# Kernel tuning notes

Measured on AMD Instinct MI355X. Metric: run time of the kernel, lower is better.

Reference implementation:

```python
import jax, jax.numpy as jnp
import numpy as np

B, L, D, H = 2, 4096, 512, 8
DK = D // H
SCALE = 1.0 / float(np.sqrt(DK))


def setup_inputs() -> dict:
    key = jax.random.key(0)
    k1, k2, k3 = jax.random.split(key, 3)
    x = jax.random.normal(k1, (B, L, D), dtype=jnp.float32)
    w_qkv = jax.random.normal(k2, (3 * D, D), dtype=jnp.float32) * 0.02
    w_o = jax.random.normal(k3, (D, D), dtype=jnp.float32) * 0.02
    return {"x": x, "w_qkv": w_qkv, "w_o": w_o}


def reference(x, w_qkv, w_o):
    b, l, d = x.shape
    # qkv projection: Linear(d, 3d, bias=False) -> x @ W^T
    qkv = (x @ w_qkv.T).reshape(b, l, 3, H, DK).transpose(2, 0, 3, 1, 4)  # [3,B,H,L,dk]
    q, k, v = qkv[0], qkv[1], qkv[2]
    # naive O(L^2) attention (faithful to source)
    scores = jnp.einsum("bhld,bhmd->bhlm", q, k) * SCALE  # [B,H,L,L]
    attn = jax.nn.softmax(scores, axis=-1)
    ctx = jnp.einsum("bhlm,bhmd->bhld", attn, v)  # [B,H,L,dk]
    ctx = ctx.transpose(0, 2, 1, 3).reshape(b, l, d)
    return ctx @ w_o.T
```

## Files before the change

kernel.cpp:

```cpp
#include <hip/hip_runtime.h>


#define Bq 2
#define Lq 4096
#define Dq 512
#define Hq 8
#define DKq 64
#define PST 40

using short8  = __attribute__((ext_vector_type(8))) short;
using ushort8 = __attribute__((ext_vector_type(8))) unsigned short;
using float4v = __attribute__((ext_vector_type(4))) float;
using half4   = __attribute__((ext_vector_type(4))) _Float16;
typedef unsigned short u16;
typedef unsigned int   u32;

__device__ __forceinline__ u16 f2bf(float f) {
    u32 u = __float_as_uint(f);
    u += 0x7fffu + ((u >> 16) & 1u);
    return (u16)(u >> 16);
}

__device__ __forceinline__ float4v mfma16(short8 a, short8 b, float4v c) {
    return __builtin_amdgcn_mfma_f32_16x16x32_bf16(a, b, c, 0, 0, 0);
}

__device__ __forceinline__ void gload_lds16(const u16* g, u16* l) {
    __builtin_amdgcn_global_load_lds(
        (const __attribute__((address_space(1))) unsigned int*)g,
        (__attribute__((address_space(3))) unsigned int*)l,
        16, 0, 0);
}

__global__ __launch_bounds__(256) void castall(const float* __restrict__ x,
                                               const float* __restrict__ wq,
                                               const float* __restrict__ wo,
                                               u16* __restrict__ xb,
                                               u16* __restrict__ wqb,
                                               u16* __restrict__ wob) {
    int g = blockIdx.x;
    const float* s; u16* d; int base;
    if (g < 4096)      { s = x;  d = xb;  base = g * 1024; }
    else if (g < 4864) { s = wq; d = wqb; base = (g - 4096) * 1024; }
    else               { s = wo; d = wob; base = (g - 4864) * 1024; }
    int i = base + threadIdx.x * 4;
    float4 f = *(const float4*)&s[i];
    ushort4 o;
    o.x = f2bf(f.x); o.y = f2bf(f.y); o.z = f2bf(f.z); o.w = f2bf(f.w);
    *(ushort4*)&d[i] = o;
}

__global__ __launch_bounds__(256) void qkv_gemm(const u16* __restrict__ A,
                                                const u16* __restrict__ Bw,
                                                u16* __restrict__ qb,
                                                u16* __restrict__ kb,
                                                u16* __restrict__ vt) {
    __shared__ __align__(16) union {
        struct { u16 A[128 * 64]; u16 B[128 * 64]; } s;
        u16 epi[128 * 134];
    } sm;
    const int m0 = blockIdx.x * 128, n0 = blockIdx.y * 128;
    const int tid = threadIdx.x, w = tid >> 6, lane = tid & 63;
    const int l15 = lane & 15, quad = lane >> 4;
    const int wy = w & 1, wx = w >> 1;
    const int r8 = lane >> 3, c8 = lane & 7, csw = c8 ^ r8;
    const int sw = l15 & 7;

    float4v acc[4][4];
    float4v zero = {0.f, 0.f, 0.f, 0.f};
#pragma unroll
    for (int mi = 0; mi < 4; mi++)
#pragma unroll
        for (int ni = 0; ni < 4; ni++) acc[mi][ni] = zero;

    for (int k0 = 0; k0 < 512; k0 += 64) {
#pragma unroll
        for (int i = 0; i < 4; i++) {
            int row = w * 32 + i * 8;
            gload_lds16(&A[(size_t)(m0 + row + r8) * 512 + k0 + csw * 8], &sm.s.A[row * 64]);
            gload_lds16(&Bw[(size_t)(n0 + row + r8) * 512 + k0 + csw * 8], &sm.s.B[row * 64]);
        }
        __syncthreads();
        short8 af0[4], af1[4], bf0[4], bf1[4];
#pragma unroll
        for (int t = 0; t < 4; t++) {
            int rowA = wy * 64 + t * 16 + l15;
            af0[t] = *(const short8*)&sm.s.A[rowA * 64 + ((quad ^ sw) * 8)];
            af1[t] = *(const short8*)&sm.s.A[rowA * 64 + (((quad + 4) ^ sw) * 8)];
            int rowB = wx * 64 + t * 16 + l15;
            bf0[t] = *(const short8*)&sm.s.B[rowB * 64 + ((quad ^ sw) * 8)];
            bf1[t] = *(const short8*)&sm.s.B[rowB * 64 + (((quad + 4) ^ sw) * 8)];
        }
#pragma unroll
        for (int mi = 0; mi < 4; mi++)
#pragma unroll
            for (int ni = 0; ni < 4; ni++) {
                acc[mi][ni] = mfma16(af0[mi], bf0[ni], acc[mi][ni]);
                acc[mi][ni] = mfma16(af1[mi], bf1[ni], acc[mi][ni]);
            }
        __syncthreads();
    }

    const int sel = n0 >> 9;
    if (sel < 2) {
        const float sc = (sel == 0) ? 0.125f : 1.0f;
#pragma unroll
        for (int mi = 0; mi < 4; mi++)
#pragma unroll
            for (int ni = 0; ni < 4; ni++)
#pragma unroll
                for (int r = 0; r < 4; r++)
                    sm.epi[(wy * 64 + mi * 16 + quad * 4 + r) * 134 + wx * 64 + ni * 16 + l15] =
                        f2bf(acc[mi][ni][r] * sc);
        __syncthreads();
        u16* tgt = (sel == 0) ? qb : kb;
#pragma unroll
        for (int i = 0; i < 8; i++) {
            int flat = i * 2048 + tid * 8;
            int row = flat >> 7, col = flat & 127;
            ushort8 vv = *(const ushort8*)&sm.epi[row * 134 + col];
            int dg = (n0 & 511) + col, h = dg >> 6, dk = dg & 63;
            int mm = m0 + row, b = mm >> 12, l = mm & 4095;
            *(ushort8*)&tgt[((size_t)(b * Hq + h) * Lq + l) * DKq + dk] = vv;
        }
    } else {
#pragma unroll
        for (int mi = 0; mi < 4; mi++)
#pragma unroll
            for (int ni = 0; ni < 4; ni++) {
                ushort4 v4;
                v4.x = f2bf(acc[mi][ni][0]); v4.y = f2bf(acc[mi][ni][1]);
                v4.z = f2bf(acc[mi][ni][2]); v4.w = f2bf(acc[mi][ni][3]);
                *(ushort4*)&sm.epi[(wx * 64 + ni * 16 + l15) * 134 + wy * 64 + mi * 16 + quad * 4] = v4;
            }
        __syncthreads();
#pragma unroll
        for (int i = 0; i < 8; i++) {
            int flat = i * 2048 + tid * 8;
            int vrow = flat >> 7, vcol = flat & 127;
            ushort8 vv = *(const ushort8*)&sm.epi[vrow * 134 + vcol];
            int dg = (n0 & 511) + vrow, h = dg >> 6, dk = dg & 63;
            int mm = m0 + vcol, b = mm >> 12, l = mm & 4095;
            *(ushort8*)&vt[((size_t)(b * Hq + h) * DKq + dk) * Lq + l] = vv;
        }
    }
}

__global__ __launch_bounds__(256, 3) void attn_kern(const u16* __restrict__ qb,
                                                    const u16* __restrict__ kb,
                                                    const u16* __restrict__ vt,
                                                    _Float16* __restrict__ op0,
                                                    _Float16* __restrict__ op1,
                                                    float* __restrict__ denp) {
    __shared__ __align__(16) u16 KV[2][2][64 * 64];
    __shared__ __align__(16) u16 Ps[4][64 * PST];
    const int g = blockIdx.x;
    const int bh = (g & 7) * 2 + ((g >> 3) & 1);
    const int rest = g >> 4;
    const int split = rest & 1;
    const int q0 = (rest >> 1) * 128;
    const int tid = threadIdx.x;
    const int w = tid >> 6, lane = tid & 63, l15 = lane & 15, quad = lane >> 4;
    const int wq = w & 1, wk = w >> 1;
    const int r8 = lane >> 3, c8 = lane & 7, csw = c8 ^ r8;
    const int sw = l15 & 7;

    const u16* qbase = qb + (size_t)bh * Lq * DKq;
    const u16* kbase = kb + (size_t)bh * Lq * DKq;
    const u16* vbase = vt + (size_t)bh * DKq * Lq;

    short8 aq0[4], aq1[4];
#pragma unroll
    for (int s = 0; s < 4; s++) {
        int qrow = q0 + wq * 64 + s * 16 + l15;
        aq0[s] = *(const short8*)&qbase[(size_t)qrow * DKq + quad * 8];
        aq1[s] = *(const short8*)&qbase[(size_t)qrow * DKq + 32 + quad * 8];
    }

    short8 ones8;
#pragma unroll
    for (int j = 0; j < 8; j++) ones8[j] = (short)0x3F80;

    float4v zero = {0.f, 0.f, 0.f, 0.f};
    float4v oacc[4][4], den[4];
#pragma unroll
    for (int s = 0; s < 4; s++) {
        den[s] = zero;
#pragma unroll
        for (int n = 0; n < 4; n++) oacc[s][n] = zero;
    }

    u16* Pw = &Ps[w][0];
    const int j0base = split * 2048;

    {
        int j0 = j0base;
        if (w < 2) {
#pragma unroll
            for (int i = 0; i < 4; i++) {
                int base = w * 32 + i * 8;
                gload_lds16(&kbase[(size_t)(j0 + base + r8) * DKq + csw * 8], &KV[0][0][base * 64]);
            }
        } else {
#pragma unroll
            for (int i = 0; i < 4; i++) {
                int base = (w - 2) * 32 + i * 8;
                gload_lds16(&vbase[(size_t)(base + r8) * Lq + j0 + csw * 8], &KV[0][1][base * 64]);
            }
        }
    }

    int p = 0;
    for (int jt = 0; jt < 32; jt++) {
        __syncthreads();
        if (jt < 31) {
            int j0 = j0base + (jt + 1) * 64;
            if (w < 2) {
#pragma unroll
                for (int i = 0; i < 4; i++) {
                    int base = w * 32 + i * 8;
                    gload_lds16(&kbase[(size_t)(j0 + base + r8) * DKq + csw * 8], &KV[p ^ 1][0][base * 64]);
                }
            } else {
#pragma unroll
                for (int i = 0; i < 4; i++) {
                    int base = (w - 2) * 32 + i * 8;
                    gload_lds16(&vbase[(size_t)(base + r8) * Lq + j0 + csw * 8], &KV[p ^ 1][1][base * 64]);
                }
            }
        }
        const u16* Kb = KV[p][0];
        const u16* Vb = KV[p][1];

#pragma unroll
        for (int kg = 0; kg < 2; kg++) {
            int krow = wk * 32 + kg * 16 + l15;
            short8 k0 = *(const short8*)&Kb[krow * 64 + ((quad ^ sw) * 8)];
            short8 k1 = *(const short8*)&Kb[krow * 64 + (((quad + 4) ^ sw) * 8)];
#pragma unroll
            for (int s = 0; s < 4; s++) {
                float4v sv = mfma16(k0, aq0[s], zero);
                sv = mfma16(k1, aq1[s], sv);
                u32 u0 = __float_as_uint(__expf(sv[0])) + 0x8000u;
                u32 u1 = __float_as_uint(__expf(sv[1])) + 0x8000u;
                u32 u2 = __float_as_uint(__expf(sv[2])) + 0x8000u;
                u32 u3 = __float_as_uint(__expf(sv[3])) + 0x8000u;
                uint2 pv;
                pv.x = __builtin_amdgcn_perm(u1, u0, 0x07060302u);
                pv.y = __builtin_amdgcn_perm(u3, u2, 0x07060302u);
                *(uint2*)&Pw[(s * 16 + l15) * PST + kg * 16 + quad * 4] = pv;
            }
        }

        short8 vf[4];
#pragma unroll
        for (int n = 0; n < 4; n++)
            vf[n] = *(const short8*)&Vb[(n * 16 + l15) * 64 + (((wk * 4 + quad) ^ sw) * 8)];
#pragma unroll
        for (int s = 0; s < 4; s++) {
            short8 ap = *(const short8*)&Pw[(s * 16 + l15) * PST + quad * 8];
            den[s] = mfma16(ap, ones8, den[s]);
#pragma unroll
            for (int n = 0; n < 4; n++)
                oacc[s][n] = mfma16(ap, vf[n], oacc[s][n]);
        }
        p ^= 1;
    }
    __syncthreads();

    float4v* sc4 = (float4v*)&KV[0][0][0];
    if (wk == 1) {
        float4v* dst = sc4 + (size_t)(wq * 64 + lane) * 12;
#pragma unroll
        for (int s = 0; s < 4; s++) dst[s] = den[s];
#pragma unroll
        for (int s = 0; s < 2; s++)
#pragma unroll
            for (int n = 0; n < 4; n++) dst[4 + s * 4 + n] = oacc[s][n];
    }
    __syncthreads();
    if (wk == 0) {
        float4v* src = sc4 + (size_t)(wq * 64 + lane) * 12;
#pragma unroll
        for (int s = 0; s < 4; s++) den[s] += src[s];
#pragma unroll
        for (int s = 0; s < 2; s++)
#pragma unroll
            for (int n = 0; n < 4; n++) oacc[s][n] += src[4 + s * 4 + n];
    }
    __syncthreads();
    if (wk == 1) {
        float4v* dst = sc4 + (size_t)(wq * 64 + lane) * 8;
#pragma unroll
        for (int s = 2; s < 4; s++)
#pragma unroll
            for (int n = 0; n < 4; n++) dst[(s - 2) * 4 + n] = oacc[s][n];
    }
    __syncthreads();
    if (wk == 0) {
        float4v* src = sc4 + (size_t)(wq * 64 + lane) * 8;
#pragma unroll
        for (int s = 2; s < 4; s++)
#pragma unroll
            for (int n = 0; n < 4; n++) oacc[s][n] += src[(s - 2) * 4 + n];

        _Float16* op = split ? op1 : op0;
#pragma unroll
        for (int s = 0; s < 4; s++)
#pragma unroll
            for (int r = 0; r < 4; r++) {
                float dv = den[s][r];
                float rd = __builtin_amdgcn_rcpf(dv);
                int row = q0 + wq * 64 + s * 16 + quad * 4 + r;
                if (l15 == 0) denp[(size_t)(split * 16 + bh) * Lq + row] = dv;
#pragma unroll
                for (int n = 0; n < 4; n++)
                    op[((size_t)bh * Lq + row) * DKq + n * 16 + l15] =
                        (_Float16)(oacc[s][n][r] * rd);
            }
    }
}

__global__ __launch_bounds__(256) void combine(const _Float16* __restrict__ op0,
                                               const _Float16* __restrict__ op1,
                                               const float* __restrict__ denp,
                                               u16* __restrict__ ctxq) {
    int t = blockIdx.x * 256 + threadIdx.x;
    int dk4 = t & 15, l = (t >> 4) & 4095, bh = t >> 16;
    size_t r0 = (size_t)bh * Lq + l;
    half4 h0 = *(const half4*)&op0[r0 * DKq + dk4 * 4];
    half4 h1 = *(const half4*)&op1[r0 * DKq + dk4 * 4];
    float d0 = denp[r0];
    float d1 = denp[(size_t)(16 + bh) * Lq + l];
    float rs = __builtin_amdgcn_rcpf(d0 + d1);
    int b = bh >> 3, h = bh & 7;
    ushort4 o;
    o.x = f2bf(((float)h0.x * d0 + (float)h1.x * d1) * rs);
    o.y = f2bf(((float)h0.y * d0 + (float)h1.y * d1) * rs);
    o.z = f2bf(((float)h0.z * d0 + (float)h1.z * d1) * rs);
    o.w = f2bf(((float)h0.w * d0 + (float)h1.w * d1) * rs);
    *(ushort4*)&ctxq[((size_t)(b * Lq + l)) * Dq + h * DKq + dk4 * 4] = o;
}

__global__ __launch_bounds__(256) void out_gemm(const u16* __restrict__ A,
                                                const u16* __restrict__ Bw,
                                                float* __restrict__ out) {
    __shared__ __align__(16) union {
        struct { u16 A[128 * 64]; u16 B[128 * 64]; } s;
        float fepi[64 * 132];
    } sm;
    const int m0 = blockIdx.x * 128, n0 = blockIdx.y * 128;
    const int tid = threadIdx.x, w = tid >> 6, lane = tid & 63;
    const int l15 = lane & 15, quad = lane >> 4;
    const int wy = w & 1, wx = w >> 1;
    const int r8 = lane >> 3, c8 = lane & 7, csw = c8 ^ r8;
    const int sw = l15 & 7;

    float4v acc[4][4];
    float4v zero = {0.f, 0.f, 0.f, 0.f};
#pragma unroll
    for (int mi = 0; mi < 4; mi++)
#pragma unroll
        for (int ni = 0; ni < 4; ni++) acc[mi][ni] = zero;

    for (int k0 = 0; k0 < 512; k0 += 64) {
#pragma unroll
        for (int i = 0; i < 4; i++) {
            int row = w * 32 + i * 8;
            gload_lds16(&A[(size_t)(m0 + row + r8) * 512 + k0 + csw * 8], &sm.s.A[row * 64]);
            gload_lds16(&Bw[(size_t)(n0 + row + r8) * 512 + k0 + csw * 8], &sm.s.B[row * 64]);
        }
        __syncthreads();
        short8 af0[4], af1[4], bf0[4], bf1[4];
#pragma unroll
        for (int t = 0; t < 4; t++) {
            int rowA = wy * 64 + t * 16 + l15;
            af0[t] = *(const short8*)&sm.s.A[rowA * 64 + ((quad ^ sw) * 8)];
            af1[t] = *(const short8*)&sm.s.A[rowA * 64 + (((quad + 4) ^ sw) * 8)];
            int rowB = wx * 64 + t * 16 + l15;
            bf0[t] = *(const short8*)&sm.s.B[rowB * 64 + ((quad ^ sw) * 8)];
            bf1[t] = *(const short8*)&sm.s.B[rowB * 64 + (((quad + 4) ^ sw) * 8)];
        }
#pragma unroll
        for (int mi = 0; mi < 4; mi++)
#pragma unroll
            for (int ni = 0; ni < 4; ni++) {
                acc[mi][ni] = mfma16(af0[mi], bf0[ni], acc[mi][ni]);
                acc[mi][ni] = mfma16(af1[mi], bf1[ni], acc[mi][ni]);
            }
        __syncthreads();
    }

#pragma unroll
    for (int ph = 0; ph < 2; ph++) {
#pragma unroll
        for (int mh = 0; mh < 2; mh++) {
            int mi = ph * 2 + mh;
            int lr = wy * 32 + mh * 16 + quad * 4;
#pragma unroll
            for (int ni = 0; ni < 4; ni++)
#pragma unroll
                for (int r = 0; r < 4; r++)
                    sm.fepi[(lr + r) * 132 + wx * 64 + ni * 16 + l15] = acc[mi][ni][r];
        }
        __syncthreads();
#pragma unroll
        for (int i = 0; i < 8; i++) {
            int flat = i * 1024 + tid * 4;
            int lrow = flat >> 7, col = flat & 127;
            float4 vv = *(const float4*)&sm.fepi[lrow * 132 + col];
            int m = (lrow & 31) + (lrow >> 5) * 64 + ph * 32;
            *(float4*)&out[(size_t)(m0 + m) * 512 + n0 + col] = vv;
        }
        __syncthreads();
    }
}

extern "C" void kernel_launch(void* const* d_in, const int* in_sizes, int n_in,
                              void* d_out, int out_size, void* d_ws, size_t ws_size,
                              hipStream_t stream) {
    const float* x     = (const float*)d_in[0];
    const float* w_qkv = (const float*)d_in[1];
    const float* w_o   = (const float*)d_in[2];
    float* out = (float*)d_out;

    const size_t N_X   = (size_t)Bq * Lq * Dq;
    const size_t N_WQ  = (size_t)3 * Dq * Dq;
    const size_t N_WO  = (size_t)Dq * Dq;
    const size_t N_QKV = (size_t)Bq * Hq * Lq * DKq;

    u16* xb  = (u16*)d_ws;
    u16* wqb = xb + N_X;
    u16* wob = wqb + N_WQ;
    u16* qb  = wob + N_WO;
    u16* kb  = qb + N_QKV;
    u16* vt  = kb + N_QKV;
    u16* o1r = vt + N_QKV;

    _Float16* op0  = (_Float16*)xb;
    _Float16* op1  = (_Float16*)o1r;
    float*    denp = (float*)wqb;
    u16*      ctxq = qb;

    castall<<<dim3(5120), 256, 0, stream>>>(x, w_qkv, w_o, xb, wqb, wob);
    qkv_gemm<<<dim3(64, 12), 256, 0, stream>>>(xb, wqb, qb, kb, vt);
    attn_kern<<<dim3(1024), 256, 0, stream>>>(qb, kb, vt, op0, op1, denp);
    combine<<<dim3(4096), 256, 0, stream>>>(op0, op1, denp, ctxq);
    out_gemm<<<dim3(64, 4), 256, 0, stream>>>(ctxq, wob, out);
}
```

Before: 221.4 us.

## Single-buffer attention LDS for occupancy, use exp2 with folded scale, retile out GEMM

```diff
diff --git a/kernel.cpp b/kernel.cpp
--- a/kernel.cpp
+++ b/kernel.cpp
@@ -19,6 +19,14 @@
     u32 u = __float_as_uint(f);
     u += 0x7fffu + ((u >> 16) & 1u);
     return (u16)(u >> 16);
+}
+
+__device__ __forceinline__ float exp2fast(float x) {
+#if __has_builtin(__builtin_amdgcn_exp2f)
+    return __builtin_amdgcn_exp2f(x);
+#else
+    return exp2f(x);
+#endif
 }
 
 __device__ __forceinline__ float4v mfma16(short8 a, short8 b, float4v c) {
@@ -103,7 +111,7 @@
 
     const int sel = n0 >> 9;
     if (sel < 2) {
-        const float sc = (sel == 0) ? 0.125f : 1.0f;
+        const float sc = (sel == 0) ? 0.18033688f : 1.0f;
 #pragma unroll
         for (int mi = 0; mi < 4; mi++)
 #pragma unroll
@@ -146,17 +154,19 @@
     }
 }
 
-__global__ __launch_bounds__(256, 3) void attn_kern(const u16* __restrict__ qb,
+__global__ __launch_bounds__(256, 4) void attn_kern(const u16* __restrict__ qb,
                                                     const u16* __restrict__ kb,
                                                     const u16* __restrict__ vt,
                                                     _Float16* __restrict__ op0,
                                                     _Float16* __restrict__ op1,
                                                     float* __restrict__ denp) {
-    __shared__ __align__(16) u16 KV[2][2][64 * 64];
-    __shared__ __align__(16) u16 Ps[4][64 * PST];
+    __shared__ __align__(16) u16 SM[18432];
+    u16* Ks = SM;
+    u16* Vs = SM + 4096;
     const int g = blockIdx.x;
-    const int bh = (g & 7) * 2 + ((g >> 3) & 1);
-    const int rest = g >> 4;
+    const int xcd = g & 7, idx = g >> 3;
+    const int bh = xcd * 2 + (idx & 1);
+    const int rest = idx >> 1;
     const int split = rest & 1;
     const int q0 = (rest >> 1) * 128;
     const int tid = threadIdx.x;
@@ -164,6 +174,7 @@
     const int wq = w & 1, wk = w >> 1;
     const int r8 = lane >> 3, c8 = lane & 7, csw = c8 ^ r8;
     const int sw = l15 & 7;
+    u16* Pw = SM + 8192 + w * 64 * PST;
 
     const u16* qbase = qb + (size_t)bh * Lq * DKq;
     const u16* kbase = kb + (size_t)bh * Lq * DKq;
@@ -190,61 +201,43 @@
         for (int n = 0; n < 4; n++) oacc[s][n] = zero;
     }
 
-    u16* Pw = &Ps[w][0];
     const int j0base = split * 2048;
 
-    {
-        int j0 = j0base;
+    for (int jt = 0; jt < 32; jt++) {
+        int j0 = j0base + jt * 64;
         if (w < 2) {
 #pragma unroll
             for (int i = 0; i < 4; i++) {
                 int base = w * 32 + i * 8;
-                gload_lds16(&kbase[(size_t)(j0 + base + r8) * DKq + csw * 8], &KV[0][0][base * 64]);
+                gload_lds16(&kbase[(size_t)(j0 + base + r8) * DKq + csw * 8], &Ks[base * 64]);
             }
         } else {
 #pragma unroll
             for (int i = 0; i < 4; i++) {
                 int base = (w - 2) * 32 + i * 8;
-                gload_lds16(&vbase[(size_t)(base + r8) * Lq + j0 + csw * 8], &KV[0][1][base * 64]);
-            }
-        }
-    }
-
-    int p = 0;
-    for (int jt = 0; jt < 32; jt++) {
-        __syncthreads();
-        if (jt < 31) {
-            int j0 = j0base + (jt + 1) * 64;
-            if (w < 2) {
-#pragma unroll
-                for (int i = 0; i < 4; i++) {
-                    int base = w * 32 + i * 8;
-                    gload_lds16(&kbase[(size_t)(j0 + base + r8) * DKq + csw * 8], &KV[p ^ 1][0][base * 64]);
-                }
-            } else {
-#pragma unroll
-                for (int i = 0; i < 4; i++) {
-                    int base = (w - 2) * 32 + i * 8;
-                    gload_lds16(&vbase[(size_t)(base + r8) * Lq + j0 + csw * 8], &KV[p ^ 1][1][base * 64]);
-                }
-            }
-        }
-        const u16* Kb = KV[p][0];
-        const u16* Vb = KV[p][1];
+                gload_lds16(&vbase[(size_t)(base + r8) * Lq + j0 + csw * 8], &Vs[base * 64]);
+            }
+        }
+        __syncthreads();
+
+        short8 vf[4];
+#pragma unroll
+        for (int n = 0; n < 4; n++)
+            vf[n] = *(const short8*)&Vs[(n * 16 + l15) * 64 + (((wk * 4 + quad) ^ sw) * 8)];
 
 #pragma unroll
         for (int kg = 0; kg < 2; kg++) {
             int krow = wk * 32 + kg * 16 + l15;
-            short8 k0 = *(const short8*)&Kb[krow * 64 + ((quad ^ sw) * 8)];
-            short8 k1 = *(const short8*)&Kb[krow * 64 + (((quad + 4) ^ sw) * 8)];
+            short8 k0 = *(const short8*)&Ks[krow * 64 + ((quad ^ sw) * 8)];
+            short8 k1 = *(const short8*)&Ks[krow * 64 + (((quad + 4) ^ sw) * 8)];
 #pragma unroll
             for (int s = 0; s < 4; s++) {
                 float4v sv = mfma16(k0, aq0[s], zero);
                 sv = mfma16(k1, aq1[s], sv);
-                u32 u0 = __float_as_uint(__expf(sv[0])) + 0x8000u;
-                u32 u1 = __float_as_uint(__expf(sv[1])) + 0x8000u;
-                u32 u2 = __float_as_uint(__expf(sv[2])) + 0x8000u;
-                u32 u3 = __float_as_uint(__expf(sv[3])) + 0x8000u;
+                u32 u0 = __float_as_uint(exp2fast(sv[0])) + 0x8000u;
+                u32 u1 = __float_as_uint(exp2fast(sv[1])) + 0x8000u;
+                u32 u2 = __float_as_uint(exp2fast(sv[2])) + 0x8000u;
+                u32 u3 = __float_as_uint(exp2fast(sv[3])) + 0x8000u;
                 uint2 pv;
                 pv.x = __builtin_amdgcn_perm(u1, u0, 0x07060302u);
                 pv.y = __builtin_amdgcn_perm(u3, u2, 0x07060302u);
@@ -252,10 +245,6 @@
             }
         }
 
-        short8 vf[4];
-#pragma unroll
-        for (int n = 0; n < 4; n++)
-            vf[n] = *(const short8*)&Vb[(n * 16 + l15) * 64 + (((wk * 4 + quad) ^ sw) * 8)];
 #pragma unroll
         for (int s = 0; s < 4; s++) {
             short8 ap = *(const short8*)&Pw[(s * 16 + l15) * PST + quad * 8];
@@ -264,11 +253,10 @@
             for (int n = 0; n < 4; n++)
                 oacc[s][n] = mfma16(ap, vf[n], oacc[s][n]);
         }
-        p ^= 1;
-    }
-    __syncthreads();
-
-    float4v* sc4 = (float4v*)&KV[0][0][0];
+        __syncthreads();
+    }
+
+    float4v* sc4 = (float4v*)SM;
     if (wk == 1) {
         float4v* dst = sc4 + (size_t)(wq * 64 + lane) * 12;
 #pragma unroll
@@ -346,45 +334,52 @@
                                                 const u16* __restrict__ Bw,
                                                 float* __restrict__ out) {
     __shared__ __align__(16) union {
-        struct { u16 A[128 * 64]; u16 B[128 * 64]; } s;
-        float fepi[64 * 132];
+        struct { u16 A[128 * 64]; u16 B[64 * 64]; } s;
+        float fepi[64 * 68];
     } sm;
-    const int m0 = blockIdx.x * 128, n0 = blockIdx.y * 128;
+    const int m0 = blockIdx.x * 128, n0 = blockIdx.y * 64;
     const int tid = threadIdx.x, w = tid >> 6, lane = tid & 63;
     const int l15 = lane & 15, quad = lane >> 4;
-    const int wy = w & 1, wx = w >> 1;
+    const int wy = w & 1, wx = (w >> 1) & 1;
     const int r8 = lane >> 3, c8 = lane & 7, csw = c8 ^ r8;
     const int sw = l15 & 7;
 
-    float4v acc[4][4];
+    float4v acc[4][2];
     float4v zero = {0.f, 0.f, 0.f, 0.f};
 #pragma unroll
     for (int mi = 0; mi < 4; mi++)
 #pragma unroll
-        for (int ni = 0; ni < 4; ni++) acc[mi][ni] = zero;
+        for (int ni = 0; ni < 2; ni++) acc[mi][ni] = zero;
 
     for (int k0 = 0; k0 < 512; k0 += 64) {
 #pragma unroll
         for (int i = 0; i < 4; i++) {
             int row = w * 32 + i * 8;
             gload_lds16(&A[(size_t)(m0 + row + r8) * 512 + k0 + csw * 8], &sm.s.A[row * 64]);
+        }
+#pragma unroll
+        for (int i = 0; i < 2; i++) {
+            int row = w * 16 + i * 8;
             gload_lds16(&Bw[(size_t)(n0 + row + r8) * 512 + k0 + csw * 8], &sm.s.B[row * 64]);
         }
         __syncthreads();
-        short8 af0[4], af1[4], bf0[4], bf1[4];
+        short8 af0[4], af1[4], bf0[2], bf1[2];
 #pragma unroll
         for (int t = 0; t < 4; t++) {
             int rowA = wy * 64 + t * 16 + l15;
             af0[t] = *(const short8*)&sm.s.A[rowA * 64 + ((quad ^ sw) * 8)];
             af1[t] = *(const short8*)&sm.s.A[rowA * 64 + (((quad + 4) ^ sw) * 8)];
-            int rowB = wx * 64 + t * 16 + l15;
+        }
+#pragma unroll
+        for (int t = 0; t < 2; t++) {
+            int rowB = wx * 32 + t * 16 + l15;
             bf0[t] = *(const short8*)&sm.s.B[rowB * 64 + ((quad ^ sw) * 8)];
             bf1[t] = *(const short8*)&sm.s.B[rowB * 64 + (((quad + 4) ^ sw) * 8)];
         }
 #pragma unroll
         for (int mi = 0; mi < 4; mi++)
 #pragma unroll
-            for (int ni = 0; ni < 4; ni++) {
+            for (int ni = 0; ni < 2; ni++) {
                 acc[mi][ni] = mfma16(af0[mi], bf0[ni], acc[mi][ni]);
                 acc[mi][ni] = mfma16(af1[mi], bf1[ni], acc[mi][ni]);
             }
@@ -398,17 +393,17 @@
             int mi = ph * 2 + mh;
             int lr = wy * 32 + mh * 16 + quad * 4;
 #pragma unroll
-            for (int ni = 0; ni < 4; ni++)
+            for (int ni = 0; ni < 2; ni++)
 #pragma unroll
                 for (int r = 0; r < 4; r++)
-                    sm.fepi[(lr + r) * 132 + wx * 64 + ni * 16 + l15] = acc[mi][ni][r];
-        }
-        __syncthreads();
-#pragma unroll
-        for (int i = 0; i < 8; i++) {
+                    sm.fepi[(lr + r) * 68 + wx * 32 + ni * 16 + l15] = acc[mi][ni][r];
+        }
+        __syncthreads();
+#pragma unroll
+        for (int i = 0; i < 4; i++) {
             int flat = i * 1024 + tid * 4;
-            int lrow = flat >> 7, col = flat & 127;
-            float4 vv = *(const float4*)&sm.fepi[lrow * 132 + col];
+            int lrow = flat >> 6, col = flat & 63;
+            float4 vv = *(const float4*)&sm.fepi[lrow * 68 + col];
             int m = (lrow & 31) + (lrow >> 5) * 64 + ph * 32;
             *(float4*)&out[(size_t)(m0 + m) * 512 + n0 + col] = vv;
         }
@@ -446,5 +441,5 @@
     qkv_gemm<<<dim3(64, 12), 256, 0, stream>>>(xb, wqb, qb, kb, vt);
     attn_kern<<<dim3(1024), 256, 0, stream>>>(qb, kb, vt, op0, op1, denp);
     combine<<<dim3(4096), 256, 0, stream>>>(op0, op1, denp, ctxq);
-    out_gemm<<<dim3(64, 4), 256, 0, stream>>>(ctxq, wob, out);
-}
+    out_gemm<<<dim3(64, 8), 256, 0, stream>>>(ctxq, wob, out);
+}
```

Result: slower. 613.4 us (+177.1%).
